# Kernel tuning notes

Hardware: AMD Instinct MI355X
Metric: run time of the kernel (lower is better)

Reference implementation:

```python
import jax, jax.numpy as jnp
import numpy as np

B, S, D, H = 8, 512, 2048, 16
DOWN, UP, R = 512, 2048, 512
HD = D // H        # 128, used only in the additive scale
VHD = UP // H      # 128, content head dim / value head dim
BASE = 10000.0


def _rope_tables(head_dim):
    # Faithful to source: positions span arange(head_dim), NOT max_len.
    pos = jnp.arange(head_dim, dtype=jnp.float32)
    div = jnp.exp(jnp.arange(0, head_dim, 2, dtype=jnp.float32) * (-np.log(BASE) / head_dim))
    theta = jnp.outer(pos, div)          # [head_dim, head_dim//2]
    return jnp.sin(theta), jnp.cos(theta)


def _apply_rope(q, num_heads, head_dim):
    # q: [B, S, num_heads*head_dim] -> [B, num_heads, S, head_dim] with interleaved rotation
    b, s, _ = q.shape
    q = q.reshape(b, s, num_heads, head_dim).transpose(0, 2, 1, 3)
    sin, cos = _rope_tables(head_dim)
    sin = sin[:s][None, None]            # [1,1,S,head_dim//2]
    cos = cos[:s][None, None]
    q_ = q.reshape(b, num_heads, s, head_dim // 2, 2)
    q1, q2 = q_[..., 0], q_[..., 1]
    o1 = q1 * cos - q2 * sin
    o2 = q2 * cos + q1 * sin
    return jnp.stack([o1, o2], axis=-1).reshape(b, num_heads, s, head_dim)


def setup_inputs() -> dict:
    key = jax.random.key(0)
    ks = jax.random.split(key, 18)
    w = lambda k, shp: jax.random.normal(k, shp, jnp.float32) * 0.02
    return {
        "X":    jax.random.normal(ks[0], (B, S, D), jnp.float32),
        "Wdq":  w(ks[1], (D, DOWN)),      "bdq":  w(ks[2], (DOWN,)),
        "Wdkv": w(ks[3], (D, DOWN)),      "bdkv": w(ks[4], (DOWN,)),
        "Wuq":  w(ks[5], (DOWN, UP)),     "buq":  w(ks[6], (UP,)),
        "Wuk":  w(ks[7], (DOWN, UP)),     "buk":  w(ks[8], (UP,)),
        "Wuv":  w(ks[9], (DOWN, UP)),     "buv":  w(ks[10], (UP,)),
        "Wqr":  w(ks[11], (DOWN, R * H)), "bqr":  w(ks[12], (R * H,)),
        "Wkr":  w(ks[13], (D, R)),        "bkr":  w(ks[14], (R,)),
        "Wfc":  w(ks[15], (VHD * H, D)),  "bfc":  w(ks[16], (D,)),
    }


def reference(X, Wdq, bdq, Wdkv, bdkv, Wuq, buq, Wuk, buk, Wuv, buv,
              Wqr, bqr, Wkr, bkr, Wfc, bfc):
    b, s, _ = X.shape
    c_q = X @ Wdq + bdq                                  # [B,S,DOWN]
    c_kv = X @ Wdkv + bdkv                               # [B,S,DOWN]
    q_c = (c_q @ Wuq + buq).reshape(b, s, H, VHD).transpose(0, 2, 1, 3)   # [B,H,S,VHD]
    k_c = (c_kv @ Wuk + buk).reshape(b, s, H, VHD).transpose(0, 2, 1, 3)
    v_c = (c_kv @ Wuv + buv).reshape(b, s, H, VHD).transpose(0, 2, 1, 3)
    q_r = _apply_rope(c_q @ Wqr + bqr, H, R)             # [B,H,S,R]
    k_r = _apply_rope(X @ Wkr + bkr, 1, R)               # [B,1,S,R]
    q = jnp.concatenate([q_c, q_r], axis=-1)             # [B,H,S,VHD+R]
    k = jnp.concatenate([k_c, jnp.broadcast_to(k_r, (b, H, s, R))], axis=-1)
    scale = HD ** 0.5 + R ** 0.5                         # additive scale, as in source
    scores = jnp.einsum('bhqd,bhkd->bhqk', q, k) / scale
    attn = jax.nn.softmax(scores, axis=-1)               # dropout: eval mode (identity)
    o = jnp.einsum('bhqk,bhkd->bhqd', attn, v_c).transpose(0, 2, 1, 3).reshape(b, s, H * VHD)
    return o @ Wfc + bfc
```

## Files before the change

kernel.cpp:

```cpp
#include <hip/hip_runtime.h>
#include <hip/hip_bf16.h>
#include <stdint.h>

typedef unsigned short u16;
typedef short bf16x8 __attribute__((ext_vector_type(8)));
typedef float f32x4 __attribute__((ext_vector_type(4)));

__device__ __forceinline__ float us2f(u16 u) {
    union { unsigned int i; float f; } x;
    x.i = ((unsigned int)u) << 16;
    return x.f;
}

__device__ __forceinline__ u16 f2us(float f) {
    union { float f; unsigned int i; } x; x.f = f;
    unsigned int lsb = (x.i >> 16) & 1u;
    x.i += 0x7FFFu + lsb;
    return (u16)(x.i >> 16);
}

__device__ __forceinline__ void gl_lds16(const u16* g, u16* l) {
    __builtin_amdgcn_global_load_lds(
        (const __attribute__((address_space(1))) void*)(uintptr_t)(const void*)g,
        (__attribute__((address_space(3))) void*)(uintptr_t)(void*)l,
        16, 0, 0);
}

#define FLAG_ROPE2  1
#define FLAG_TRANS2 4
#define FLAG_F32OUT 8

struct GArgs {
    const u16 *A0, *B0, *B0r2;
    int K0;
    const float* bias;
    void* C; void* C2;
    int colSplit;
};

template <int LDA0, int LDB0, int LDC, int LDC2, int FLAGS>
__global__ __launch_bounds__(256)
void gemm_mfma(GArgs g)
{
    __shared__ u16 As[128 * 64];
    __shared__ u16 Bs[128 * 64];

    const int t    = threadIdx.x;
    const int lane = t & 63;
    const int w    = t >> 6;
    const int wm   = w >> 1, wn = w & 1;
    const int m0   = blockIdx.y * 128;
    const int n0   = blockIdx.x * 128;
    const bool r2  = (n0 >= g.colSplit);

    const int srow = t >> 3;
    const int sp   = t & 7;
    u16* dA = As + t * 8;
    u16* dB = Bs + t * 8;

    const int lr = lane & 15;
    const int jj = lane >> 4;

    f32x4 acc[4][4];
#pragma unroll
    for (int i = 0; i < 4; ++i)
#pragma unroll
        for (int j = 0; j < 4; ++j)
            acc[i][j] = (f32x4){0.f, 0.f, 0.f, 0.f};

    {
        const u16* A = g.A0;
        const u16* B = r2 ? g.B0r2 - (long)g.colSplit * LDB0 : g.B0;
        const u16* gA[4];
        const u16* gB[4];
#pragma unroll
        for (int r = 0; r < 4; ++r) {
            int row = r * 32 + srow;
            int gc  = (sp - row) & 7;
            gA[r] = A + (long)(m0 + row) * LDA0 + gc * 8;
            gB[r] = B + (long)(n0 + row) * LDB0 + gc * 8;
        }
        for (int kt = 0; kt < g.K0; kt += 64) {
#pragma unroll
            for (int r = 0; r < 4; ++r) {
                gl_lds16(gA[r], dA + r * 2048);
                gl_lds16(gB[r], dB + r * 2048);
                gA[r] += 64; gB[r] += 64;
            }
            __syncthreads();
#pragma unroll
            for (int s = 0; s < 2; ++s) {
                bf16x8 af[4], bfr[4];
#pragma unroll
                for (int mi = 0; mi < 4; ++mi) {
                    int row  = wm * 64 + mi * 16 + lr;
                    int slot = (s * 4 + jj + row) & 7;
                    af[mi] = *(const bf16x8*)&As[row * 64 + slot * 8];
                }
#pragma unroll
                for (int ni = 0; ni < 4; ++ni) {
                    int row  = wn * 64 + ni * 16 + lr;
                    int slot = (s * 4 + jj + row) & 7;
                    bfr[ni] = *(const bf16x8*)&Bs[row * 64 + slot * 8];
                }
#pragma unroll
                for (int mi = 0; mi < 4; ++mi)
#pragma unroll
                    for (int ni = 0; ni < 4; ++ni)
                        acc[mi][ni] = __builtin_amdgcn_mfma_f32_16x16x32_bf16(
                            af[mi], bfr[ni], acc[mi][ni], 0, 0, 0);
            }
            __syncthreads();
        }
    }

    const int eCol0 = n0 + wn * 64 + lr;
    const int eRow0 = m0 + wm * 64 + jj * 4;
    const bool oddc = lane & 1;

    if (g.bias) {
#pragma unroll
        for (int ni = 0; ni < 4; ++ni) {
            float bv = g.bias[eCol0 + ni * 16];
#pragma unroll
            for (int mi = 0; mi < 4; ++mi) {
                acc[mi][ni][0] += bv; acc[mi][ni][1] += bv;
                acc[mi][ni][2] += bv; acc[mi][ni][3] += bv;
            }
        }
    }

    if (!r2) {
#pragma unroll
        for (int mi = 0; mi < 4; ++mi)
#pragma unroll
            for (int ni = 0; ni < 4; ++ni) {
                int rowb = eRow0 + mi * 16;
                int colg = eCol0 + ni * 16;
                if (FLAGS & FLAG_F32OUT) {
                    float* cp = (float*)g.C;
#pragma unroll
                    for (int i = 0; i < 4; ++i)
                        cp[(long)(rowb + i) * LDC + colg] = acc[mi][ni][i];
                } else {
                    u16* cp = (u16*)g.C;
#pragma unroll
                    for (int i = 0; i < 4; ++i)
                        cp[(long)(rowb + i) * LDC + colg] = f2us(acc[mi][ni][i]);
                }
            }
    } else if (FLAGS & FLAG_ROPE2) {
        const float base_s = (float)(eRow0 & 511);
#pragma unroll
        for (int ni = 0; ni < 4; ++ni) {
            int col2 = eCol0 + ni * 16 - g.colSplit;
            int rp   = (col2 & 511) & ~1;
            float f  = __expf(-9.2103403719761836f * (float)rp * (1.0f / 512.0f));
            float s1, c1, s16, c16, sb, cb;
            __sincosf(f, &s1, &c1);
            __sincosf(16.0f * f, &s16, &c16);
            __sincosf(base_s * f, &sb, &cb);
            float cm = cb, sm = sb;
#pragma unroll
            for (int mi = 0; mi < 4; ++mi) {
                f32x4 v = acc[mi][ni];
                float cr = cm, sr = sm;
#pragma unroll
                for (int i = 0; i < 4; ++i) {
                    float other = __shfl_xor(v[i], 1, 64);
                    v[i] = oddc ? (v[i] * cr + other * sr)
                                : (v[i] * cr - other * sr);
                    float cn = cr * c1 - sr * s1;
                    sr = sr * c1 + cr * s1; cr = cn;
                }
                int rowb = eRow0 + mi * 16;
                u16* cp = (u16*)g.C2;
#pragma unroll
                for (int i = 0; i < 4; ++i)
                    cp[(long)(rowb + i) * LDC2 + col2] = f2us(v[i]);
                float cn = cm * c16 - sm * s16;
                sm = sm * c16 + cm * s16; cm = cn;
            }
        }
    } else {
#pragma unroll
        for (int mi = 0; mi < 4; ++mi)
#pragma unroll
            for (int ni = 0; ni < 4; ++ni) {
                int rowb = eRow0 + mi * 16;
                int col2 = eCol0 + ni * 16 - g.colSplit;
                if (FLAGS & FLAG_TRANS2) {
                    u16* cp = (u16*)g.C2 + (long)col2 * LDC2 + rowb;
                    ushort4 o4;
                    o4.x = f2us(acc[mi][ni][0]); o4.y = f2us(acc[mi][ni][1]);
                    o4.z = f2us(acc[mi][ni][2]); o4.w = f2us(acc[mi][ni][3]);
                    *(ushort4*)cp = o4;
                } else {
                    u16* cp = (u16*)g.C2;
#pragma unroll
                    for (int i = 0; i < 4; ++i)
                        cp[(long)(rowb + i) * LDC2 + col2] = f2us(acc[mi][ni][i]);
                }
            }
    }
}

__global__ __launch_bounds__(256, 2)
void attn_fused(const u16* __restrict__ qc, const u16* __restrict__ kc,
                const u16* __restrict__ qr, const u16* __restrict__ kr,
                const u16* __restrict__ vt, u16* __restrict__ o)
{
    __shared__ u16 As[128 * 64];
    __shared__ u16 Bs[128 * 64];
    __shared__ u16 Ps[128 * 136];
    __shared__ float l_sum[128];

    const int t    = threadIdx.x;
    const int lane = t & 63;
    const int w    = t >> 6;
    const int wm   = w >> 1, wn = w & 1;

    const int flat = blockIdx.x + (blockIdx.y << 2);
    const int xcd  = flat & 7;
    const int j    = flat >> 3;
    const int m0   = (j & 3) * 128;
    const int z    = xcd * 16 + (j >> 2);
    const int bb   = z >> 4, h = z & 15;

    if (t < 128) l_sum[t] = 0.f;

    const int srow = t >> 3;
    const int sp   = t & 7;
    u16* dA = As + t * 8;
    u16* dB = Bs + t * 8;
    int rrow[4], rgc[4];
#pragma unroll
    for (int r = 0; r < 4; ++r) {
        rrow[r] = r * 32 + srow;
        rgc[r]  = (sp - rrow[r]) & 7;
    }

    const int lr = lane & 15;
    const int jj = lane >> 4;

    const u16* gqc[4];
    const u16* gqr[4];
#pragma unroll
    for (int r = 0; r < 4; ++r) {
        gqc[r] = qc + (long)(bb * 512 + m0 + rrow[r]) * 2048 + h * 128 + rgc[r] * 8;
        gqr[r] = qr + (long)(bb * 512 + m0 + rrow[r]) * 8192 + h * 512 + rgc[r] * 8;
    }

    f32x4 acc_o[4][4];
#pragma unroll
    for (int i = 0; i < 4; ++i)
#pragma unroll
        for (int j2 = 0; j2 < 4; ++j2) acc_o[i][j2] = (f32x4){0.f, 0.f, 0.f, 0.f};

    const float scale = 1.0f / 33.941125496954285f;

    for (int nt = 0; nt < 4; ++nt) {
        const int n0k = nt * 128;

        f32x4 acc_s[4][4];
#pragma unroll
        for (int i = 0; i < 4; ++i)
#pragma unroll
            for (int j2 = 0; j2 < 4; ++j2) acc_s[i][j2] = (f32x4){0.f, 0.f, 0.f, 0.f};

        const u16* pa[4];
        const u16* pb[4];
#pragma unroll
        for (int r = 0; r < 4; ++r) {
            pa[r] = gqc[r];
            pb[r] = kc + (long)(bb * 512 + n0k + rrow[r]) * 2048 + h * 128 + rgc[r] * 8;
        }
        for (int seg = 0; seg < 2; ++seg) {
            int iters = seg == 0 ? 2 : 8;
            for (int kt = 0; kt < iters; ++kt) {
#pragma unroll
                for (int r = 0; r < 4; ++r) {
                    gl_lds16(pa[r], dA + r * 2048);
                    gl_lds16(pb[r], dB + r * 2048);
                    pa[r] += 64; pb[r] += 64;
                }
                __syncthreads();
                __builtin_amdgcn_s_setprio(1);
#pragma unroll
                for (int s = 0; s < 2; ++s) {
                    bf16x8 af[4], bfr[4];
#pragma unroll
                    for (int mi = 0; mi < 4; ++mi) {
                        int row  = wm * 64 + mi * 16 + lr;
                        int slot = (s * 4 + jj + row) & 7;
                        af[mi] = *(const bf16x8*)&As[row * 64 + slot * 8];
                    }
#pragma unroll
                    for (int ni = 0; ni < 4; ++ni) {
                        int row  = wn * 64 + ni * 16 + lr;
                        int slot = (s * 4 + jj + row) & 7;
                        bfr[ni] = *(const bf16x8*)&Bs[row * 64 + slot * 8];
                    }
#pragma unroll
                    for (int mi = 0; mi < 4; ++mi)
#pragma unroll
                        for (int ni = 0; ni < 4; ++ni)
                            acc_s[mi][ni] = __builtin_amdgcn_mfma_f32_16x16x32_bf16(
                                af[mi], bfr[ni], acc_s[mi][ni], 0, 0, 0);
                }
                __builtin_amdgcn_s_setprio(0);
                __syncthreads();
            }
            if (seg == 0) {
#pragma unroll
                for (int r = 0; r < 4; ++r) {
                    pa[r] = gqr[r];
                    pb[r] = kr + (long)(bb * 512 + n0k + rrow[r]) * 1536 + rgc[r] * 8;
                }
            }
        }

        const u16* pv[4];
#pragma unroll
        for (int r = 0; r < 4; ++r) {
            pv[r] = vt + (long)(h * 128 + rrow[r]) * 4096 + bb * 512 + n0k + rgc[r] * 8;
            gl_lds16(pv[r], dB + r * 2048);
            pv[r] += 64;
        }

#pragma unroll
        for (int mi = 0; mi < 4; ++mi) {
            float rowpart[4] = {0.f, 0.f, 0.f, 0.f};
#pragma unroll
            for (int ni = 0; ni < 4; ++ni) {
                f32x4 v = acc_s[mi][ni];
                int colP = wn * 64 + ni * 16 + lr;
#pragma unroll
                for (int i = 0; i < 4; ++i) {
                    float e = __expf(v[i] * scale);
                    rowpart[i] += e;
                    int rowP = wm * 64 + mi * 16 + jj * 4 + i;
                    Ps[rowP * 136 + colP] = f2us(e);
                }
            }
#pragma unroll
            for (int i = 0; i < 4; ++i) {
                float s4 = rowpart[i];
                s4 += __shfl_xor(s4, 1, 64);
                s4 += __shfl_xor(s4, 2, 64);
                s4 += __shfl_xor(s4, 4, 64);
                s4 += __shfl_xor(s4, 8, 64);
                if ((lane & 15) == 0)
                    atomicAdd(&l_sum[wm * 64 + mi * 16 + jj * 4 + i], s4);
            }
        }
        __syncthreads();

#pragma unroll
        for (int kt = 0; kt < 2; ++kt) {
            if (kt == 1) {
                __syncthreads();
#pragma unroll
                for (int r = 0; r < 4; ++r)
                    gl_lds16(pv[r], dB + r * 2048);
                __syncthreads();
            }
            __builtin_amdgcn_s_setprio(1);
#pragma unroll
            for (int s = 0; s < 2; ++s) {
                bf16x8 af[4], bfr[4];
#pragma unroll
                for (int mi = 0; mi < 4; ++mi) {
                    int row = wm * 64 + mi * 16 + lr;
                    af[mi] = *(const bf16x8*)&Ps[row * 136 + kt * 64 + s * 32 + jj * 8];
                }
#pragma unroll
                for (int ni = 0; ni < 4; ++ni) {
                    int row  = wn * 64 + ni * 16 + lr;
                    int slot = (s * 4 + jj + row) & 7;
                    bfr[ni] = *(const bf16x8*)&Bs[row * 64 + slot * 8];
                }
#pragma unroll
                for (int mi = 0; mi < 4; ++mi)
#pragma unroll
                    for (int ni = 0; ni < 4; ++ni)
                        acc_o[mi][ni] = __builtin_amdgcn_mfma_f32_16x16x32_bf16(
                            af[mi], bfr[ni], acc_o[mi][ni], 0, 0, 0);
            }
            __builtin_amdgcn_s_setprio(0);
        }
        __syncthreads();
    }

#pragma unroll
    for (int mi = 0; mi < 4; ++mi) {
#pragma unroll
        for (int i = 0; i < 4; ++i) {
            int row = wm * 64 + mi * 16 + jj * 4 + i;
            float linv = 1.0f / l_sum[row];
            long grow = (long)(bb * 512 + m0 + row) * 2048 + h * 128;
#pragma unroll
            for (int ni = 0; ni < 4; ++ni) {
                int colc = wn * 64 + ni * 16 + lr;
                o[grow + colc] = f2us(acc_o[mi][ni][i] * linv);
            }
        }
    }
}

__global__ __launch_bounds__(256)
void conv_f32_bf16(const float* __restrict__ in, u16* __restrict__ out)
{
    int i = blockIdx.x * 256 + threadIdx.x;
    float4 v = ((const float4*)in)[i];
    ushort4 o;
    o.x = f2us(v.x); o.y = f2us(v.y); o.z = f2us(v.z); o.w = f2us(v.w);
    ((ushort4*)out)[i] = o;
}

struct TCAll {
    const float *Wdq, *Wdkv, *Wkr, *Wuq, *Wuk, *Wuv, *Wqr, *Wfc;
    u16 *Wc1, *Wc2, *Wqr_t, *Wfc_t;
};

__global__ __launch_bounds__(256)
void tconv_all(TCAll a)
{
    __shared__ float tile[32][33];
    const int bid = blockIdx.x;
    const float* in; u16* out; int K, N, nx, ny;
    if (bid < 3072) {
        int z = bid >> 10, rem = bid & 1023;
        in = z == 0 ? a.Wdq : (z == 1 ? a.Wdkv : a.Wkr);
        out = a.Wc1 + z * 1048576;
        K = 2048; N = 512; nx = rem & 15; ny = rem >> 4;
    } else if (bid < 6144) {
        int l = bid - 3072, z = l >> 10, rem = l & 1023;
        in = z == 0 ? a.Wuq : (z == 1 ? a.Wuk : a.Wuv);
        out = a.Wc2 + z * 1048576;
        K = 512; N = 2048; nx = rem & 63; ny = rem >> 6;
    } else if (bid < 10240) {
        int l = bid - 6144;
        in = a.Wqr; out = a.Wqr_t;
        K = 512; N = 8192; nx = l & 255; ny = l >> 8;
    } else {
        int l = bid - 10240;
        in = a.Wfc; out = a.Wfc_t;
        K = 2048; N = 2048; nx = l & 63; ny = l >> 6;
    }
    const int n0 = nx * 32, k0 = ny * 32;
    const int c = threadIdx.x & 31, r0 = threadIdx.x >> 5;
#pragma unroll
    for (int j = 0; j < 4; ++j) {
        int r = r0 + j * 8;
        tile[r][c] = in[(long)(k0 + r) * N + n0 + c];
    }
    __syncthreads();
#pragma unroll
    for (int j = 0; j < 4; ++j) {
        int r = r0 + j * 8;
        out[(long)(n0 + r) * K + k0 + c] = f2us(tile[c][r]);
    }
}

struct BG {
    const float *bdq, *bdkv, *bkr, *buq, *bqr, *buk, *buv;
    float *biasD, *biasQ, *biasK;
};

__global__ __launch_bounds__(256)
void bias_gather(BG a)
{
    int i = blockIdx.x * 256 + threadIdx.x;
    if (i < 1536) {
        float v = i < 512 ? a.bdq[i] : (i < 1024 ? a.bdkv[i - 512] : a.bkr[i - 1024]);
        a.biasD[i] = v;
    } else if (i < 11776) {
        int j = i - 1536;
        a.biasQ[j] = j < 2048 ? a.buq[j] : a.bqr[j - 2048];
    } else {
        int j = i - 11776;
        a.biasK[j] = j < 2048 ? a.buk[j] : a.buv[j - 2048];
    }
}

extern "C" void kernel_launch(void* const* d_in, const int* in_sizes, int n_in,
                              void* d_out, int out_size, void* d_ws, size_t ws_size,
                              hipStream_t stream)
{
    (void)in_sizes; (void)n_in; (void)out_size; (void)ws_size;

    const float* X    = (const float*)d_in[0];
    const float* Wdq  = (const float*)d_in[1];  const float* bdq  = (const float*)d_in[2];
    const float* Wdkv = (const float*)d_in[3];  const float* bdkv = (const float*)d_in[4];
    const float* Wuq  = (const float*)d_in[5];  const float* buq  = (const float*)d_in[6];
    const float* Wuk  = (const float*)d_in[7];  const float* buk  = (const float*)d_in[8];
    const float* Wuv  = (const float*)d_in[9];  const float* buv  = (const float*)d_in[10];
    const float* Wqr  = (const float*)d_in[11]; const float* bqr  = (const float*)d_in[12];
    const float* Wkr  = (const float*)d_in[13]; const float* bkr  = (const float*)d_in[14];
    const float* Wfc  = (const float*)d_in[15]; const float* bfc  = (const float*)d_in[16];
    float* out = (float*)d_out;

    u16* ws = (u16*)d_ws;
    u16* Xb     = ws;
    u16* Wc1    = Xb   + 8388608;
    u16* Wc2    = Wc1  + 3145728;
    u16* Wqr_t  = Wc2  + 3145728;
    u16* Wfc_t  = Wqr_t + 4194304;
    u16* ckk    = Wfc_t + 4194304;
    u16* q_c    = ckk  + 6291456;
    u16* k_c    = q_c  + 8388608;
    u16* v_t    = k_c  + 8388608;
    u16* q_r    = v_t  + 8388608;
    u16* o      = q_r  + 33554432;
    float* biasD = (float*)(o + 8388608);
    float* biasQ = biasD + 1536;
    float* biasK = biasQ + 10240;

    dim3 blk(256, 1, 1);

    conv_f32_bf16<<<8192, blk, 0, stream>>>(X, Xb);
    {   TCAll a{Wdq, Wdkv, Wkr, Wuq, Wuk, Wuv, Wqr, Wfc,
                Wc1, Wc2, Wqr_t, Wfc_t};
        tconv_all<<<14336, blk, 0, stream>>>(a); }
    {   BG a{bdq, bdkv, bkr, buq, bqr, buk, buv, biasD, biasQ, biasK};
        bias_gather<<<62, blk, 0, stream>>>(a); }

    const int NOSPLIT = 1 << 30;

    {
        GArgs a{};
        a.A0 = Xb; a.B0 = Wc1; a.B0r2 = Wc1 + 2l * 1048576; a.K0 = 2048;
        a.bias = biasD; a.C = ckk; a.C2 = ckk + 1024;
        a.colSplit = 1024;
        gemm_mfma<2048, 2048, 1536, 1536, FLAG_ROPE2>
            <<<dim3(12, 32, 1), blk, 0, stream>>>(a);
    }
    {
        GArgs a{};
        a.A0 = ckk; a.B0 = Wc2; a.B0r2 = Wqr_t; a.K0 = 512;
        a.bias = biasQ; a.C = q_c; a.C2 = q_r;
        a.colSplit = 2048;
        gemm_mfma<1536, 512, 2048, 8192, FLAG_ROPE2>
            <<<dim3(80, 32, 1), blk, 0, stream>>>(a);
    }
    {
        GArgs a{};
        a.A0 = ckk + 512; a.B0 = Wc2 + 1048576; a.B0r2 = Wc2 + 2l * 1048576;
        a.K0 = 512;
        a.bias = biasK; a.C = k_c; a.C2 = v_t;
        a.colSplit = 2048;
        gemm_mfma<1536, 512, 2048, 4096, FLAG_TRANS2>
            <<<dim3(32, 32, 1), blk, 0, stream>>>(a);
    }

    attn_fused<<<dim3(4, 128, 1), blk, 0, stream>>>(
        q_c, k_c, q_r, ckk + 1024, v_t, o);

    {
        GArgs a{};
        a.A0 = o; a.B0 = Wfc_t; a.B0r2 = Wfc_t; a.K0 = 2048;
        a.bias = bfc; a.C = out; a.C2 = out;
        a.colSplit = NOSPLIT;
        gemm_mfma<2048, 2048, 2048, 1, FLAG_F32OUT>
            <<<dim3(16, 32, 1), blk, 0, stream>>>(a);
    }
}
```

Measured before the change: 429.8 us.

## Widen attention K-tiles to 128 and stage V fully in a separate LDS region

```diff
diff --git a/kernel.cpp b/kernel.cpp
--- a/kernel.cpp
+++ b/kernel.cpp
@@ -210,10 +210,13 @@
                 const u16* __restrict__ qr, const u16* __restrict__ kr,
                 const u16* __restrict__ vt, u16* __restrict__ o)
 {
-    __shared__ u16 As[128 * 64];
-    __shared__ u16 Bs[128 * 64];
-    __shared__ u16 Ps[128 * 136];
+    __shared__ u16 sbuf[33792];
     __shared__ float l_sum[128];
+
+    u16* As = sbuf;
+    u16* Bs = sbuf + 16384;
+    u16* Ps = sbuf;
+    u16* Vs = sbuf + 17408;
 
     const int t    = threadIdx.x;
     const int lane = t & 63;
@@ -229,27 +232,18 @@
 
     if (t < 128) l_sum[t] = 0.f;
 
-    const int srow = t >> 3;
-    const int sp   = t & 7;
+    const int srow = t >> 4;
+    const int sp   = t & 15;
+    const int gc   = (sp - srow) & 15;
     u16* dA = As + t * 8;
     u16* dB = Bs + t * 8;
-    int rrow[4], rgc[4];
-#pragma unroll
-    for (int r = 0; r < 4; ++r) {
-        rrow[r] = r * 32 + srow;
-        rgc[r]  = (sp - rrow[r]) & 7;
-    }
+    u16* dV = Vs + t * 8;
 
     const int lr = lane & 15;
     const int jj = lane >> 4;
 
-    const u16* gqc[4];
-    const u16* gqr[4];
-#pragma unroll
-    for (int r = 0; r < 4; ++r) {
-        gqc[r] = qc + (long)(bb * 512 + m0 + rrow[r]) * 2048 + h * 128 + rgc[r] * 8;
-        gqr[r] = qr + (long)(bb * 512 + m0 + rrow[r]) * 8192 + h * 512 + rgc[r] * 8;
-    }
+    const u16* qcB = qc + (long)(bb * 512 + m0 + srow) * 2048 + h * 128 + gc * 8;
+    const u16* qrB = qr + (long)(bb * 512 + m0 + srow) * 8192 + h * 512 + gc * 8;
 
     f32x4 acc_o[4][4];
 #pragma unroll
@@ -268,65 +262,79 @@
 #pragma unroll
             for (int j2 = 0; j2 < 4; ++j2) acc_s[i][j2] = (f32x4){0.f, 0.f, 0.f, 0.f};
 
-        const u16* pa[4];
-        const u16* pb[4];
-#pragma unroll
-        for (int r = 0; r < 4; ++r) {
-            pa[r] = gqc[r];
-            pb[r] = kc + (long)(bb * 512 + n0k + rrow[r]) * 2048 + h * 128 + rgc[r] * 8;
-        }
-        for (int seg = 0; seg < 2; ++seg) {
-            int iters = seg == 0 ? 2 : 8;
-            for (int kt = 0; kt < iters; ++kt) {
-#pragma unroll
-                for (int r = 0; r < 4; ++r) {
-                    gl_lds16(pa[r], dA + r * 2048);
-                    gl_lds16(pb[r], dB + r * 2048);
-                    pa[r] += 64; pb[r] += 64;
-                }
-                __syncthreads();
-                __builtin_amdgcn_s_setprio(1);
-#pragma unroll
-                for (int s = 0; s < 2; ++s) {
-                    bf16x8 af[4], bfr[4];
-#pragma unroll
-                    for (int mi = 0; mi < 4; ++mi) {
-                        int row  = wm * 64 + mi * 16 + lr;
-                        int slot = (s * 4 + jj + row) & 7;
-                        af[mi] = *(const bf16x8*)&As[row * 64 + slot * 8];
-                    }
-#pragma unroll
-                    for (int ni = 0; ni < 4; ++ni) {
-                        int row  = wn * 64 + ni * 16 + lr;
-                        int slot = (s * 4 + jj + row) & 7;
-                        bfr[ni] = *(const bf16x8*)&Bs[row * 64 + slot * 8];
-                    }
-#pragma unroll
-                    for (int mi = 0; mi < 4; ++mi)
-#pragma unroll
-                        for (int ni = 0; ni < 4; ++ni)
-                            acc_s[mi][ni] = __builtin_amdgcn_mfma_f32_16x16x32_bf16(
-                                af[mi], bfr[ni], acc_s[mi][ni], 0, 0, 0);
-                }
-                __builtin_amdgcn_s_setprio(0);
-                __syncthreads();
-            }
-            if (seg == 0) {
-#pragma unroll
-                for (int r = 0; r < 4; ++r) {
-                    pa[r] = gqr[r];
-                    pb[r] = kr + (long)(bb * 512 + n0k + rrow[r]) * 1536 + rgc[r] * 8;
-                }
-            }
-        }
-
-        const u16* pv[4];
-#pragma unroll
-        for (int r = 0; r < 4; ++r) {
-            pv[r] = vt + (long)(h * 128 + rrow[r]) * 4096 + bb * 512 + n0k + rgc[r] * 8;
-            gl_lds16(pv[r], dB + r * 2048);
-            pv[r] += 64;
-        }
+        const u16* kcB = kc + (long)(bb * 512 + n0k + srow) * 2048 + h * 128 + gc * 8;
+        const u16* krB = kr + (long)(bb * 512 + n0k + srow) * 1536 + gc * 8;
+
+#pragma unroll
+        for (int r = 0; r < 8; ++r) {
+            gl_lds16(qcB + r * 32768, dA + r * 2048);
+            gl_lds16(kcB + r * 32768, dB + r * 2048);
+        }
+        __syncthreads();
+        __builtin_amdgcn_s_setprio(1);
+#pragma unroll
+        for (int s = 0; s < 4; ++s) {
+            bf16x8 af[4], bfr[4];
+#pragma unroll
+            for (int mi = 0; mi < 4; ++mi) {
+                int row  = wm * 64 + mi * 16 + lr;
+                int slot = (s * 4 + jj + row) & 15;
+                af[mi] = *(const bf16x8*)&As[row * 128 + slot * 8];
+            }
+#pragma unroll
+            for (int ni = 0; ni < 4; ++ni) {
+                int row  = wn * 64 + ni * 16 + lr;
+                int slot = (s * 4 + jj + row) & 15;
+                bfr[ni] = *(const bf16x8*)&Bs[row * 128 + slot * 8];
+            }
+#pragma unroll
+            for (int mi = 0; mi < 4; ++mi)
+#pragma unroll
+                for (int ni = 0; ni < 4; ++ni)
+                    acc_s[mi][ni] = __builtin_amdgcn_mfma_f32_16x16x32_bf16(
+                        af[mi], bfr[ni], acc_s[mi][ni], 0, 0, 0);
+        }
+        __builtin_amdgcn_s_setprio(0);
+        __syncthreads();
+
+        for (int kt = 0; kt < 4; ++kt) {
+#pragma unroll
+            for (int r = 0; r < 8; ++r) {
+                gl_lds16(qrB + kt * 128 + r * 131072, dA + r * 2048);
+                gl_lds16(krB + kt * 128 + r * 24576,  dB + r * 2048);
+            }
+            __syncthreads();
+            __builtin_amdgcn_s_setprio(1);
+#pragma unroll
+            for (int s = 0; s < 4; ++s) {
+                bf16x8 af[4], bfr[4];
+#pragma unroll
+                for (int mi = 0; mi < 4; ++mi) {
+                    int row  = wm * 64 + mi * 16 + lr;
+                    int slot = (s * 4 + jj + row) & 15;
+                    af[mi] = *(const bf16x8*)&As[row * 128 + slot * 8];
+                }
+#pragma unroll
+                for (int ni = 0; ni < 4; ++ni) {
+                    int row  = wn * 64 + ni * 16 + lr;
+                    int slot = (s * 4 + jj + row) & 15;
+                    bfr[ni] = *(const bf16x8*)&Bs[row * 128 + slot * 8];
+                }
+#pragma unroll
+                for (int mi = 0; mi < 4; ++mi)
+#pragma unroll
+                    for (int ni = 0; ni < 4; ++ni)
+                        acc_s[mi][ni] = __builtin_amdgcn_mfma_f32_16x16x32_bf16(
+                            af[mi], bfr[ni], acc_s[mi][ni], 0, 0, 0);
+            }
+            __builtin_amdgcn_s_setprio(0);
+            __syncthreads();
+        }
+
+        const u16* vtB = vt + (long)(h * 128 + srow) * 4096 + bb * 512 + n0k + gc * 8;
+#pragma unroll
+        for (int r = 0; r < 8; ++r)
+            gl_lds16(vtB + r * 65536, dV + r * 2048);
 
 #pragma unroll
         for (int mi = 0; mi < 4; ++mi) {
@@ -356,39 +364,29 @@
         }
         __syncthreads();
 
-#pragma unroll
-        for (int kt = 0; kt < 2; ++kt) {
-            if (kt == 1) {
-                __syncthreads();
-#pragma unroll
-                for (int r = 0; r < 4; ++r)
-                    gl_lds16(pv[r], dB + r * 2048);
-                __syncthreads();
-            }
-            __builtin_amdgcn_s_setprio(1);
-#pragma unroll
-            for (int s = 0; s < 2; ++s) {
-                bf16x8 af[4], bfr[4];
-#pragma unroll
-                for (int mi = 0; mi < 4; ++mi) {
-                    int row = wm * 64 + mi * 16 + lr;
-                    af[mi] = *(const bf16x8*)&Ps[row * 136 + kt * 64 + s * 32 + jj * 8];
-                }
-#pragma unroll
-                for (int ni = 0; ni < 4; ++ni) {
-                    int row  = wn * 64 + ni * 16 + lr;
-                    int slot = (s * 4 + jj + row) & 7;
-                    bfr[ni] = *(const bf16x8*)&Bs[row * 64 + slot * 8];
-                }
-#pragma unroll
-                for (int mi = 0; mi < 4; ++mi)
-#pragma unroll
-                    for (int ni = 0; ni < 4; ++ni)
-                        acc_o[mi][ni] = __builtin_amdgcn_mfma_f32_16x16x32_bf16(
-                            af[mi], bfr[ni], acc_o[mi][ni], 0, 0, 0);
-            }
-            __builtin_amdgcn_s_setprio(0);
-        }
+        __builtin_amdgcn_s_setprio(1);
+#pragma unroll
+        for (int s = 0; s < 4; ++s) {
+            bf16x8 af[4], bfr[4];
+#pragma unroll
+            for (int mi = 0; mi < 4; ++mi) {
+                int row = wm * 64 + mi * 16 + lr;
+                af[mi] = *(const bf16x8*)&Ps[row * 136 + s * 32 + jj * 8];
+            }
+#pragma unroll
+            for (int ni = 0; ni < 4; ++ni) {
+                int row  = wn * 64 + ni * 16 + lr;
+                int slot = (s * 4 + jj + row) & 15;
+                bfr[ni] = *(const bf16x8*)&Vs[row * 128 + slot * 8];
+            }
+#pragma unroll
+            for (int mi = 0; mi < 4; ++mi)
+#pragma unroll
+                for (int ni = 0; ni < 4; ++ni)
+                    acc_o[mi][ni] = __builtin_amdgcn_mfma_f32_16x16x32_bf16(
+                        af[mi], bfr[ni], acc_o[mi][ni], 0, 0, 0);
+        }
+        __builtin_amdgcn_s_setprio(0);
         __syncthreads();
     }
 
```

Result: slower. 439.3 us (+2.2%).
